# Kernel tuning notes

Measured on AMD Instinct MI355X. Metric: run time of the kernel, lower is better.

## Reference

```python
import jax, jax.numpy as jnp
import numpy as np

N = 100_000   # nodes
E = 3_200_000  # edges (avg degree 32)


def setup_inputs() -> dict:
    key = jax.random.key(0)
    ks = jax.random.split(key, 8)
    x = jax.random.normal(ks[0], (N, 4), dtype=jnp.float32)
    edge_index = jax.random.randint(ks[1], (2, E), 0, N, dtype=jnp.int64)
    # GCNConv weights: lin(in,out,bias=False) then bias added post-aggregation
    W1 = jax.random.normal(ks[2], (4, 16), dtype=jnp.float32) * 0.5
    b1 = jax.random.normal(ks[3], (16,), dtype=jnp.float32) * 0.1
    W2 = jax.random.normal(ks[4], (16, 32), dtype=jnp.float32) * 0.25
    b2 = jax.random.normal(ks[5], (32,), dtype=jnp.float32) * 0.1
    Wfc = jax.random.normal(ks[6], (32, 4), dtype=jnp.float32) * 0.2
    bfc = jax.random.normal(ks[7], (4,), dtype=jnp.float32) * 0.1
    return {"x": x, "edge_index": edge_index, "W1": W1, "b1": b1,
            "W2": W2, "b2": b2, "Wfc": Wfc, "bfc": bfc}


def _gcn_conv(x, W, b, src, dst, norm):
    # h_j = x_j @ W ; out_i = sum_{j->i} norm_ij * h_j ; + bias
    n = x.shape[0]
    h = x @ W
    msg = h[src] * norm[:, None]              # [E+N, out]
    out = jax.ops.segment_sum(msg, dst, num_segments=n)
    return out + b


def reference(x, edge_index, W1, b1, W2, b2, Wfc, bfc):
    n = x.shape[0]
    loops = jnp.arange(n, dtype=edge_index.dtype)
    src = jnp.concatenate([edge_index[0], loops])  # PyG: row = source j
    dst = jnp.concatenate([edge_index[1], loops])  # col = target i
    # symmetric normalization with self-loops (PyG gcn_norm default)
    deg = jax.ops.segment_sum(jnp.ones(dst.shape[0], x.dtype), dst, num_segments=n)
    dinv = jnp.where(deg > 0, jax.lax.rsqrt(deg), jnp.zeros_like(deg))
    norm = dinv[src] * dinv[dst]

    h = jax.nn.relu(_gcn_conv(x, W1, b1, src, dst, norm))
    h = jax.nn.relu(_gcn_conv(h, W2, b2, src, dst, norm))
    return h @ Wfc + bfc
```

## Files before the change

kernel.cpp:

```cpp
#include <hip/hip_runtime.h>
#include <hip/hip_bf16.h>
#include <hip/hip_fp16.h>


#define NBUCK 1024
#define TILE  4096
#define BSH   7
#define CAP   5120

__global__ __launch_bounds__(512)
void k_bucket(const int* __restrict__ src, const int* __restrict__ dst,
              int* __restrict__ gcur, int* __restrict__ colbkt, int E) {
    __shared__ int hist[NBUCK];
    __shared__ int cur[NBUCK];
    __shared__ int scanT[512];
    __shared__ int reorder[TILE];
    int t = threadIdx.x;
    int tb = blockIdx.x * TILE;
    int cntT = min(TILE, E - tb);

    hist[t] = 0; hist[t + 512] = 0;
    __syncthreads();

    for (int i = t; i < cntT; i += 512)
        atomicAdd(&hist[dst[tb + i] >> BSH], 1);
    __syncthreads();

    int b0 = t * 2;
    int h0 = hist[b0], h1 = hist[b0 + 1];
    int s = h0 + h1;
    scanT[t] = s;
    __syncthreads();
    for (int off = 1; off < 512; off <<= 1) {
        int v = (t >= off) ? scanT[t - off] : 0;
        __syncthreads();
        scanT[t] += v;
        __syncthreads();
    }
    int ex = scanT[t] - s;
    cur[b0] = ex;
    cur[b0 + 1] = ex + h0;
    __syncthreads();

    for (int i = t; i < cntT; i += 512) {
        int sv = src[tb + i];
        int d  = dst[tb + i];
        int b  = d >> BSH;
        int r  = atomicAdd(&cur[b], 1);
        reorder[r] = sv | ((d & ((1 << BSH) - 1)) << 17);
    }
    __syncthreads();

    #pragma unroll
    for (int j = 0; j < 2; j++) {
        int b = b0 + j;
        int c = hist[b];
        if (c > 0) {
            int gb = atomicAdd(&gcur[b], c);
            int lo = cur[b] - c;
            for (int k = 0; k < c; k++) {
                int idx = gb + k;
                if (idx < CAP) colbkt[(size_t)b * CAP + idx] = reorder[lo + k];
            }
        }
    }
}

__global__ __launch_bounds__(256)
void k_sortpre(const int* __restrict__ gcur, int* __restrict__ colbkt,
               const float* __restrict__ x, float* __restrict__ dinv,
               __half* __restrict__ g1h, int* __restrict__ rowbeg,
               int* __restrict__ rowlen, int n) {
    __shared__ int recbuf[CAP];
    __shared__ int sorted[CAP];
    __shared__ int hist[128];
    __shared__ int off[128];
    __shared__ int cur[128];
    int t = threadIdx.x, b = blockIdx.x;
    int nb = min(gcur[b], CAP);
    int* row = colbkt + (size_t)b * CAP;
    if (t < 128) hist[t] = 0;
    __syncthreads();
    for (int e = t; e < nb; e += 256) {
        int rec = __builtin_nontemporal_load(row + e);
        recbuf[e] = rec;
        atomicAdd(&hist[(rec >> 17) & 127], 1);
    }
    __syncthreads();
    if (t < 128) off[t] = hist[t];
    __syncthreads();
    for (int d = 1; d < 128; d <<= 1) {
        int v = 0;
        if (t < 128 && t >= d) v = off[t - d];
        __syncthreads();
        if (t < 128) off[t] += v;
        __syncthreads();
    }
    if (t < 128) cur[t] = off[t] - hist[t];
    __syncthreads();
    for (int e = t; e < nb; e += 256) {
        int rec = recbuf[e];
        int dl = (rec >> 17) & 127;
        int p = atomicAdd(&cur[dl], 1);
        sorted[p] = rec;
    }
    __syncthreads();
    for (int e = t; e < nb; e += 256)
        __builtin_nontemporal_store(sorted[e], row + e);
    if (t < 128) {
        int node = (b << BSH) + t;
        if (node < n) {
            int len = hist[t];
            rowlen[node] = len;
            rowbeg[node] = b * CAP + (off[t] - len);
            float di = rsqrtf((float)len + 1.0f);
            dinv[node] = di;
            float4 xv = *reinterpret_cast<const float4*>(x + (size_t)node * 4);
            union { __half2 h2[2]; uint2 u2; } pk;
            pk.h2[0] = __floats2half2_rn(di * xv.x, di * xv.y);
            pk.h2[1] = __floats2half2_rn(di * xv.z, di * xv.w);
            *reinterpret_cast<uint2*>(g1h + (size_t)node * 4) = pk.u2;
        }
    }
}

__device__ __forceinline__ void add_g1(float& a0, float& a1, float& a2, float& a3,
                                       uint2 u) {
    float2 f0 = __half22float2(*reinterpret_cast<const __half2*>(&u.x));
    float2 f1 = __half22float2(*reinterpret_cast<const __half2*>(&u.y));
    a0 += f0.x; a1 += f0.y; a2 += f1.x; a3 += f1.y;
}

__global__ __launch_bounds__(256)
void k_gather1(const int* __restrict__ rowbeg, const int* __restrict__ rowlen,
               const int* __restrict__ colbkt, const __half* __restrict__ g1h,
               const float* __restrict__ dinv, const float* __restrict__ W1,
               const float* __restrict__ b1, __half* __restrict__ g2h, int n) {
    __shared__ float w[64];
    __shared__ float bb[16];
    if (threadIdx.x < 64) w[threadIdx.x] = W1[threadIdx.x];
    if (threadIdx.x >= 64 && threadIdx.x < 80) bb[threadIdx.x - 64] = b1[threadIdx.x - 64];
    __syncthreads();
    int gt = blockIdx.x * 256 + threadIdx.x;
    int i = gt >> 2;
    int lane = gt & 3;
    if (i >= n) return;
    int len = rowlen[i];
    const int* row = colbkt + rowbeg[i];
    const uint2* g1v = reinterpret_cast<const uint2*>(g1h);
    float a0 = 0.f, a1 = 0.f, a2 = 0.f, a3 = 0.f;
    if (lane == 0)
        add_g1(a0, a1, a2, a3, g1v[i]);
    int e = lane;
    for (; e + 12 < len; e += 16) {
        int r0 = __builtin_nontemporal_load(row + e);
        int r1 = __builtin_nontemporal_load(row + e + 4);
        int r2 = __builtin_nontemporal_load(row + e + 8);
        int r3 = __builtin_nontemporal_load(row + e + 12);
        uint2 u0 = g1v[r0 & 0x1FFFF];
        uint2 u1 = g1v[r1 & 0x1FFFF];
        uint2 u2 = g1v[r2 & 0x1FFFF];
        uint2 u3 = g1v[r3 & 0x1FFFF];
        add_g1(a0, a1, a2, a3, u0);
        add_g1(a0, a1, a2, a3, u1);
        add_g1(a0, a1, a2, a3, u2);
        add_g1(a0, a1, a2, a3, u3);
    }
    for (; e < len; e += 4) {
        int rec = __builtin_nontemporal_load(row + e);
        add_g1(a0, a1, a2, a3, g1v[rec & 0x1FFFF]);
    }
    a0 += __shfl_xor(a0, 1); a1 += __shfl_xor(a1, 1);
    a2 += __shfl_xor(a2, 1); a3 += __shfl_xor(a3, 1);
    a0 += __shfl_xor(a0, 2); a1 += __shfl_xor(a1, 2);
    a2 += __shfl_xor(a2, 2); a3 += __shfl_xor(a3, 2);
    if (lane != 0) return;
    float di = dinv[i];
    a0 *= di; a1 *= di; a2 *= di; a3 *= di;
    union { __half2 h2[8]; uint4 u4[2]; } pk;
    #pragma unroll
    for (int c = 0; c < 8; c++) {
        int f0 = 2 * c, f1 = 2 * c + 1;
        float r0 = di * fmaxf(a0*w[f0] + a1*w[16+f0] + a2*w[32+f0] + a3*w[48+f0] + bb[f0], 0.f);
        float r1 = di * fmaxf(a0*w[f1] + a1*w[16+f1] + a2*w[32+f1] + a3*w[48+f1] + bb[f1], 0.f);
        pk.h2[c] = __floats2half2_rn(r0, r1);
    }
    uint4* o = reinterpret_cast<uint4*>(g2h + (size_t)i * 16);
    o[0] = pk.u4[0];
    o[1] = pk.u4[1];
}

__device__ __forceinline__ void add_g2(float* acc, uint4 a, uint4 b) {
    const __half2* pa = reinterpret_cast<const __half2*>(&a);
    const __half2* pb = reinterpret_cast<const __half2*>(&b);
    #pragma unroll
    for (int j = 0; j < 4; j++) {
        float2 f = __half22float2(pa[j]);
        acc[2*j] += f.x; acc[2*j+1] += f.y;
    }
    #pragma unroll
    for (int j = 0; j < 4; j++) {
        float2 f = __half22float2(pb[j]);
        acc[8+2*j] += f.x; acc[8+2*j+1] += f.y;
    }
}

__global__ __launch_bounds__(256)
void k_gather2(const int* __restrict__ rowbeg, const int* __restrict__ rowlen,
               const int* __restrict__ colbkt, const __half* __restrict__ g2h,
               const float* __restrict__ dinv, const float* __restrict__ W2,
               const float* __restrict__ b2, const float* __restrict__ Wfc,
               const float* __restrict__ bfc, float* __restrict__ out, int n) {
    __shared__ float w2[512];
    __shared__ float wf[128];
    __shared__ float b2s[32];
    __shared__ float bfs[4];
    for (int j = threadIdx.x; j < 512; j += blockDim.x) w2[j] = W2[j];
    if (threadIdx.x < 128) wf[threadIdx.x] = Wfc[threadIdx.x];
    if (threadIdx.x >= 128 && threadIdx.x < 160) b2s[threadIdx.x - 128] = b2[threadIdx.x - 128];
    if (threadIdx.x >= 160 && threadIdx.x < 164) bfs[threadIdx.x - 160] = bfc[threadIdx.x - 160];
    __syncthreads();

    int gt = blockIdx.x * 256 + threadIdx.x;
    int i = gt >> 2;
    int lane = gt & 3;
    if (i >= n) return;
    int len = rowlen[i];
    const int* row = colbkt + rowbeg[i];
    const uint4* g2v = reinterpret_cast<const uint4*>(g2h);

    float acc[16];
    #pragma unroll
    for (int k = 0; k < 16; k++) acc[k] = 0.f;
    if (lane == 0)
        add_g2(acc, g2v[(size_t)i * 2], g2v[(size_t)i * 2 + 1]);
    int e = lane;
    for (; e + 12 < len; e += 16) {
        int r0 = __builtin_nontemporal_load(row + e);
        int r1 = __builtin_nontemporal_load(row + e + 4);
        int r2 = __builtin_nontemporal_load(row + e + 8);
        int r3 = __builtin_nontemporal_load(row + e + 12);
        size_t s0 = (size_t)(r0 & 0x1FFFF) * 2;
        size_t s1 = (size_t)(r1 & 0x1FFFF) * 2;
        size_t s2 = (size_t)(r2 & 0x1FFFF) * 2;
        size_t s3 = (size_t)(r3 & 0x1FFFF) * 2;
        uint4 a0 = g2v[s0], b0 = g2v[s0 + 1];
        uint4 a1 = g2v[s1], b1 = g2v[s1 + 1];
        uint4 a2 = g2v[s2], b2v_ = g2v[s2 + 1];
        uint4 a3 = g2v[s3], b3 = g2v[s3 + 1];
        add_g2(acc, a0, b0);
        add_g2(acc, a1, b1);
        add_g2(acc, a2, b2v_);
        add_g2(acc, a3, b3);
    }
    for (; e < len; e += 4) {
        int rec = __builtin_nontemporal_load(row + e);
        size_t s = (size_t)(rec & 0x1FFFF) * 2;
        add_g2(acc, g2v[s], g2v[s + 1]);
    }
    #pragma unroll
    for (int k = 0; k < 16; k++) acc[k] += __shfl_xor(acc[k], 1);
    #pragma unroll
    for (int k = 0; k < 16; k++) acc[k] += __shfl_xor(acc[k], 2);

    float di = dinv[i];
    #pragma unroll
    for (int k = 0; k < 16; k++) acc[k] *= di;

    float o0 = (lane == 0) ? bfs[0] : 0.f;
    float o1 = (lane == 0) ? bfs[1] : 0.f;
    float o2 = (lane == 0) ? bfs[2] : 0.f;
    float o3 = (lane == 0) ? bfs[3] : 0.f;
    int fbase = lane * 8;
    #pragma unroll
    for (int fo = 0; fo < 8; fo++) {
        int f = fbase + fo;
        float h = b2s[f];
        #pragma unroll
        for (int k = 0; k < 16; k++) h += acc[k] * w2[k * 32 + f];
        h = fmaxf(h, 0.0f);
        o0 += h * wf[f * 4 + 0];
        o1 += h * wf[f * 4 + 1];
        o2 += h * wf[f * 4 + 2];
        o3 += h * wf[f * 4 + 3];
    }
    o0 += __shfl_xor(o0, 1); o1 += __shfl_xor(o1, 1);
    o2 += __shfl_xor(o2, 1); o3 += __shfl_xor(o3, 1);
    o0 += __shfl_xor(o0, 2); o1 += __shfl_xor(o1, 2);
    o2 += __shfl_xor(o2, 2); o3 += __shfl_xor(o3, 2);
    if (lane != 0) return;
    float4 r; r.x = o0; r.y = o1; r.z = o2; r.w = o3;
    *reinterpret_cast<float4*>(out + (size_t)i * 4) = r;
}

extern "C" void kernel_launch(void* const* d_in, const int* in_sizes, int n_in,
                              void* d_out, int out_size, void* d_ws, size_t ws_size,
                              hipStream_t stream) {
    const float* x   = (const float*)d_in[0];
    const int*   ei  = (const int*)d_in[1];
    const float* W1  = (const float*)d_in[2];
    const float* b1  = (const float*)d_in[3];
    const float* W2  = (const float*)d_in[4];
    const float* b2  = (const float*)d_in[5];
    const float* Wfc = (const float*)d_in[6];
    const float* bfc = (const float*)d_in[7];
    float* out = (float*)d_out;

    const int n = in_sizes[0] / 4;
    const int E = in_sizes[1] / 2;
    const int* src = ei;
    const int* dst = ei + E;

    char* p = (char*)d_ws;
    int*    gcur   = (int*)p;           p += (size_t)NBUCK * 4;
    int*    colbkt = (int*)p;           p += (size_t)NBUCK * CAP * 4;
    int*    rowbeg = (int*)p;           p += (size_t)n * 4;
    int*    rowlen = (int*)p;           p += (size_t)n * 4;
    float*  dinv   = (float*)p;         p += (size_t)n * 4;
    __half* g1h    = (__half*)p;        p += (size_t)n * 8;
    __half* g2h    = (__half*)p;        p += (size_t)n * 32;

    const int NBu = (n + 127) >> BSH;
    const int gT  = (E + TILE - 1) / TILE;
    const int gN4 = ((size_t)n * 4 + 255) / 256;

    hipMemsetAsync(gcur, 0, (size_t)NBUCK * sizeof(int), stream);

    k_bucket <<<gT,  512, 0, stream>>>(src, dst, gcur, colbkt, E);
    k_sortpre<<<NBu, 256, 0, stream>>>(gcur, colbkt, x, dinv, g1h, rowbeg, rowlen, n);
    k_gather1<<<gN4, 256, 0, stream>>>(rowbeg, rowlen, colbkt, g1h, dinv, W1, b1, g2h, n);
    k_gather2<<<gN4, 256, 0, stream>>>(rowbeg, rowlen, colbkt, g2h, dinv,
                                       W2, b2, Wfc, bfc, out, n);
}
```

Measured before the change: 144.4 us.

## Use wave-shuffle scans, register-cached edges, and 8 lanes per node in gather2

The bucket kernel now loads each thread's src/dst values once into registers (EPT=8) and reuses them for both the histogram and scatter passes, so the second global read is gone. The block-wide shared-memory Hillis-Steele scans in both k_bucket and k_sortpre become wavefront __shfl_up scans with a small cross-wave fixup, removing many __syncthreads. k_gather2 assigns 8 lanes per node instead of 4, adding parallelism for the memory-bound neighbor gather at the cost of an extra shuffle-reduction round and more threads. Register pressure rises in k_bucket from the 16 cached values.

Result: faster. 139.8 us (-3.2%).

```diff
diff --git a/kernel.cpp b/kernel.cpp
--- a/kernel.cpp
+++ b/kernel.cpp
@@ -5,6 +5,7 @@
 
 #define NBUCK 1024
 #define TILE  4096
+#define EPT   8
 #define BSH   7
 #define CAP   5120
 
@@ -13,7 +14,7 @@
               int* __restrict__ gcur, int* __restrict__ colbkt, int E) {
     __shared__ int hist[NBUCK];
     __shared__ int cur[NBUCK];
-    __shared__ int scanT[512];
+    __shared__ int scanW[8];
     __shared__ int reorder[TILE];
     int t = threadIdx.x;
     int tb = blockIdx.x * TILE;
@@ -22,32 +23,45 @@
     hist[t] = 0; hist[t + 512] = 0;
     __syncthreads();
 
-    for (int i = t; i < cntT; i += 512)
-        atomicAdd(&hist[dst[tb + i] >> BSH], 1);
+    int sv[EPT], dv[EPT];
+    #pragma unroll
+    for (int j = 0; j < EPT; j++) {
+        int i = t + j * 512;
+        bool ok = i < cntT;
+        sv[j] = ok ? src[tb + i] : 0;
+        dv[j] = ok ? dst[tb + i] : 0;
+        if (ok) atomicAdd(&hist[dv[j] >> BSH], 1);
+    }
     __syncthreads();
 
     int b0 = t * 2;
     int h0 = hist[b0], h1 = hist[b0 + 1];
     int s = h0 + h1;
-    scanT[t] = s;
-    __syncthreads();
-    for (int off = 1; off < 512; off <<= 1) {
-        int v = (t >= off) ? scanT[t - off] : 0;
-        __syncthreads();
-        scanT[t] += v;
-        __syncthreads();
-    }
-    int ex = scanT[t] - s;
+    int lane = t & 63, wid = t >> 6;
+    int incl = s;
+    #pragma unroll
+    for (int off = 1; off < 64; off <<= 1) {
+        int v = __shfl_up(incl, off);
+        if (lane >= off) incl += v;
+    }
+    if (lane == 63) scanW[wid] = incl;
+    __syncthreads();
+    int wbase = 0;
+    #pragma unroll
+    for (int wI = 0; wI < 8; wI++) wbase += (wI < wid) ? scanW[wI] : 0;
+    int ex = wbase + incl - s;
     cur[b0] = ex;
     cur[b0 + 1] = ex + h0;
     __syncthreads();
 
-    for (int i = t; i < cntT; i += 512) {
-        int sv = src[tb + i];
-        int d  = dst[tb + i];
-        int b  = d >> BSH;
-        int r  = atomicAdd(&cur[b], 1);
-        reorder[r] = sv | ((d & ((1 << BSH) - 1)) << 17);
+    #pragma unroll
+    for (int j = 0; j < EPT; j++) {
+        int i = t + j * 512;
+        if (i < cntT) {
+            int b = dv[j] >> BSH;
+            int r = atomicAdd(&cur[b], 1);
+            reorder[r] = sv[j] | ((dv[j] & ((1 << BSH) - 1)) << 17);
+        }
     }
     __syncthreads();
 
@@ -74,8 +88,9 @@
     __shared__ int recbuf[CAP];
     __shared__ int sorted[CAP];
     __shared__ int hist[128];
-    __shared__ int off[128];
+    __shared__ int offs[128];
     __shared__ int cur[128];
+    __shared__ int wtot;
     int t = threadIdx.x, b = blockIdx.x;
     int nb = min(gcur[b], CAP);
     int* row = colbkt + (size_t)b * CAP;
@@ -87,16 +102,21 @@
         atomicAdd(&hist[(rec >> 17) & 127], 1);
     }
     __syncthreads();
-    if (t < 128) off[t] = hist[t];
-    __syncthreads();
-    for (int d = 1; d < 128; d <<= 1) {
-        int v = 0;
-        if (t < 128 && t >= d) v = off[t - d];
-        __syncthreads();
-        if (t < 128) off[t] += v;
-        __syncthreads();
-    }
-    if (t < 128) cur[t] = off[t] - hist[t];
+    int h = (t < 128) ? hist[t] : 0;
+    int lane = t & 63;
+    int incl = h;
+    #pragma unroll
+    for (int off = 1; off < 64; off <<= 1) {
+        int v = __shfl_up(incl, off);
+        if (lane >= off) incl += v;
+    }
+    if (t == 63) wtot = incl;
+    __syncthreads();
+    if (t < 128) {
+        int incl2 = incl + ((t >= 64) ? wtot : 0);
+        offs[t] = incl2;
+        cur[t] = incl2 - h;
+    }
     __syncthreads();
     for (int e = t; e < nb; e += 256) {
         int rec = recbuf[e];
@@ -112,7 +132,7 @@
         if (node < n) {
             int len = hist[t];
             rowlen[node] = len;
-            rowbeg[node] = b * CAP + (off[t] - len);
+            rowbeg[node] = b * CAP + (offs[t] - len);
             float di = rsqrtf((float)len + 1.0f);
             dinv[node] = di;
             float4 xv = *reinterpret_cast<const float4*>(x + (size_t)node * 4);
@@ -222,8 +242,8 @@
     __syncthreads();
 
     int gt = blockIdx.x * 256 + threadIdx.x;
-    int i = gt >> 2;
-    int lane = gt & 3;
+    int i = gt >> 3;
+    int lane = gt & 7;
     if (i >= n) return;
     int len = rowlen[i];
     const int* row = colbkt + rowbeg[i];
@@ -235,25 +255,25 @@
     if (lane == 0)
         add_g2(acc, g2v[(size_t)i * 2], g2v[(size_t)i * 2 + 1]);
     int e = lane;
-    for (; e + 12 < len; e += 16) {
+    for (; e + 24 < len; e += 32) {
         int r0 = __builtin_nontemporal_load(row + e);
-        int r1 = __builtin_nontemporal_load(row + e + 4);
-        int r2 = __builtin_nontemporal_load(row + e + 8);
-        int r3 = __builtin_nontemporal_load(row + e + 12);
+        int r1 = __builtin_nontemporal_load(row + e + 8);
+        int r2 = __builtin_nontemporal_load(row + e + 16);
+        int r3 = __builtin_nontemporal_load(row + e + 24);
         size_t s0 = (size_t)(r0 & 0x1FFFF) * 2;
         size_t s1 = (size_t)(r1 & 0x1FFFF) * 2;
         size_t s2 = (size_t)(r2 & 0x1FFFF) * 2;
         size_t s3 = (size_t)(r3 & 0x1FFFF) * 2;
-        uint4 a0 = g2v[s0], b0 = g2v[s0 + 1];
-        uint4 a1 = g2v[s1], b1 = g2v[s1 + 1];
-        uint4 a2 = g2v[s2], b2v_ = g2v[s2 + 1];
-        uint4 a3 = g2v[s3], b3 = g2v[s3 + 1];
-        add_g2(acc, a0, b0);
-        add_g2(acc, a1, b1);
-        add_g2(acc, a2, b2v_);
-        add_g2(acc, a3, b3);
-    }
-    for (; e < len; e += 4) {
+        uint4 a0 = g2v[s0], c0 = g2v[s0 + 1];
+        uint4 a1 = g2v[s1], c1 = g2v[s1 + 1];
+        uint4 a2 = g2v[s2], c2 = g2v[s2 + 1];
+        uint4 a3 = g2v[s3], c3 = g2v[s3 + 1];
+        add_g2(acc, a0, c0);
+        add_g2(acc, a1, c1);
+        add_g2(acc, a2, c2);
+        add_g2(acc, a3, c3);
+    }
+    for (; e < len; e += 8) {
         int rec = __builtin_nontemporal_load(row + e);
         size_t s = (size_t)(rec & 0x1FFFF) * 2;
         add_g2(acc, g2v[s], g2v[s + 1]);
@@ -262,6 +282,8 @@
     for (int k = 0; k < 16; k++) acc[k] += __shfl_xor(acc[k], 1);
     #pragma unroll
     for (int k = 0; k < 16; k++) acc[k] += __shfl_xor(acc[k], 2);
+    #pragma unroll
+    for (int k = 0; k < 16; k++) acc[k] += __shfl_xor(acc[k], 4);
 
     float di = dinv[i];
     #pragma unroll
@@ -271,9 +293,9 @@
     float o1 = (lane == 0) ? bfs[1] : 0.f;
     float o2 = (lane == 0) ? bfs[2] : 0.f;
     float o3 = (lane == 0) ? bfs[3] : 0.f;
-    int fbase = lane * 8;
-    #pragma unroll
-    for (int fo = 0; fo < 8; fo++) {
+    int fbase = lane * 4;
+    #pragma unroll
+    for (int fo = 0; fo < 4; fo++) {
         int f = fbase + fo;
         float h = b2s[f];
         #pragma unroll
@@ -288,6 +310,8 @@
     o2 += __shfl_xor(o2, 1); o3 += __shfl_xor(o3, 1);
     o0 += __shfl_xor(o0, 2); o1 += __shfl_xor(o1, 2);
     o2 += __shfl_xor(o2, 2); o3 += __shfl_xor(o3, 2);
+    o0 += __shfl_xor(o0, 4); o1 += __shfl_xor(o1, 4);
+    o2 += __shfl_xor(o2, 4); o3 += __shfl_xor(o3, 4);
     if (lane != 0) return;
     float4 r; r.x = o0; r.y = o1; r.z = o2; r.w = o3;
     *reinterpret_cast<float4*>(out + (size_t)i * 4) = r;
@@ -323,12 +347,13 @@
     const int NBu = (n + 127) >> BSH;
     const int gT  = (E + TILE - 1) / TILE;
     const int gN4 = ((size_t)n * 4 + 255) / 256;
+    const int gN8 = ((size_t)n * 8 + 255) / 256;
 
     hipMemsetAsync(gcur, 0, (size_t)NBUCK * sizeof(int), stream);
 
     k_bucket <<<gT,  512, 0, stream>>>(src, dst, gcur, colbkt, E);
     k_sortpre<<<NBu, 256, 0, stream>>>(gcur, colbkt, x, dinv, g1h, rowbeg, rowlen, n);
     k_gather1<<<gN4, 256, 0, stream>>>(rowbeg, rowlen, colbkt, g1h, dinv, W1, b1, g2h, n);
-    k_gather2<<<gN4, 256, 0, stream>>>(rowbeg, rowlen, colbkt, g2h, dinv,
+    k_gather2<<<gN8, 256, 0, stream>>>(rowbeg, rowlen, colbkt, g2h, dinv,
                                        W2, b2, Wfc, bfc, out, n);
 }
```
